# Performance work log

Measured on AMD Instinct MI355X. Metric: run time of the kernel, lower is better.

The kernel has to match this reference:

```python
import jax, jax.numpy as jnp
import numpy as np

B = 8
S_MAX = 1024
H = 12
HD = 64
D = H * HD
DFF = 4 * D
NEG = -1.0e9  # matches Triton kernel's -1000000000.0 mask value


def _layernorm(x, g, b, eps=1e-6):
    mu = jnp.mean(x, axis=-1, keepdims=True)
    var = jnp.mean((x - mu) ** 2, axis=-1, keepdims=True)
    return (x - mu) * jax.lax.rsqrt(var + eps) * g + b


def setup_inputs() -> dict:
    key = jax.random.key(0)
    ks = jax.random.split(key, 12)
    lengths = np.array([1024, 896, 768, 640, 896, 1024, 512, 384], dtype=np.int32)
    assert lengths.max() <= S_MAX and len(lengths) == B
    total = int(lengths.sum())  # 6144
    cu = jnp.asarray(np.concatenate([[0], np.cumsum(lengths)]), dtype=jnp.int32)
    s = 0.02
    return {
        "x": jax.random.normal(ks[0], (total, D), jnp.float32),
        "cu_seqlens": cu,
        "g1": jnp.ones((D,), jnp.float32),
        "beta1": jnp.zeros((D,), jnp.float32),
        "Wqkv": jax.random.normal(ks[1], (D, 3 * D), jnp.float32) * s,
        "bqkv": jnp.zeros((3 * D,), jnp.float32),
        "Wo": jax.random.normal(ks[2], (D, D), jnp.float32) * s,
        "bo": jnp.zeros((D,), jnp.float32),
        "g2": jnp.ones((D,), jnp.float32),
        "beta2": jnp.zeros((D,), jnp.float32),
        "W1": jax.random.normal(ks[3], (D, DFF), jnp.float32) * s,
        "b_fc1": jnp.zeros((DFF,), jnp.float32),
        "W2": jax.random.normal(ks[4], (DFF, D), jnp.float32) * s,
        "b_fc2": jnp.zeros((D,), jnp.float32),
    }


def _ragged_attention(q, k, v, cu_seqlens):
    # q,k,v: [Total, H, HD] packed ragged sequences; cu_seqlens: [B+1] int32
    total = q.shape[0]
    lens = cu_seqlens[1:] - cu_seqlens[:-1]                      # [B]
    s = jnp.arange(S_MAX)
    pad_idx = cu_seqlens[:-1, None] + jnp.minimum(s[None, :], lens[:, None] - 1)  # [B,S]
    valid = s[None, :] < lens[:, None]                           # [B,S]
    qp = q[pad_idx]                                              # [B,S,H,HD]
    kp = k[pad_idx]
    vp = v[pad_idx]
    scale = 1.0 / jnp.sqrt(jnp.float32(HD))
    scores = jnp.einsum("bqhd,bkhd->bhqk", qp, kp) * scale      # [B,H,S,S]
    scores = jnp.where(valid[:, None, None, :], scores, NEG)     # mask invalid keys
    p = jax.nn.softmax(scores, axis=-1)
    op = jnp.einsum("bhqk,bkhd->bqhd", p, vp)                   # [B,S,H,HD]
    # repack to [Total, H, HD]
    tok = jnp.arange(total)
    seg = jnp.searchsorted(cu_seqlens, tok, side="right") - 1    # sequence id per token
    pos = tok - cu_seqlens[seg]
    return op[seg, pos]


def _forward(x, cu_seqlens, g1, beta1, Wqkv, bqkv, Wo, bo, g2, beta2, W1, b_fc1, W2, b_fc2):
    total = x.shape[0]
    qkv = (_layernorm(x, g1, beta1) @ Wqkv + bqkv).reshape(total, 3, H, HD)
    q, k, v = qkv[:, 0], qkv[:, 1], qkv[:, 2]
    attn = _ragged_attention(q, k, v, cu_seqlens).reshape(total, D)
    x = x + (attn @ Wo + bo)                                     # proj_drop/ls1/drop_path identity (eval)
    h = _layernorm(x, g2, beta2)
    m = jax.nn.gelu(h @ W1 + b_fc1, approximate=False)
    return x + (m @ W2 + b_fc2)


def reference(x, cu_seqlens, g1, beta1, Wqkv, bqkv, Wo, bo, g2, beta2, W1, b_fc1, W2, b_fc2):
    return _forward(x, cu_seqlens, g1, beta1, Wqkv, bqkv, Wo, bo, g2, beta2, W1, b_fc1, W2, b_fc2)
```

## Files before the change

kernel.cpp:

```cpp
#include <hip/hip_runtime.h>
#include <hip/hip_bf16.h>
#include <stdint.h>
#include <string.h>

#define D_MODEL 768
#define H_HEADS 12
#define HD_ 64
#define N_QKV 2304

typedef __bf16 bf16x8 __attribute__((ext_vector_type(8)));
typedef float f32x4 __attribute__((ext_vector_type(4)));

__device__ __forceinline__ unsigned short f2bfbits(float f) {
  union { float f; unsigned u; } x; x.f = f;
  unsigned r = x.u + 0x7fffu + ((x.u >> 16) & 1u);
  return (unsigned short)(r >> 16);
}

__device__ __forceinline__ unsigned pk2(float a, float b) {
  union { float f; unsigned u; } x, y; x.f = a; y.f = b;
  return ((x.u + 0x8000u) >> 16) | ((y.u + 0x8000u) & 0xffff0000u);
}

__global__ void transpose_w(const float* __restrict__ in, unsigned short* __restrict__ out,
                            int R, int C) {
  __shared__ float tile[32][33];
  int c0 = blockIdx.x * 32, r0 = blockIdx.y * 32;
  int tx = threadIdx.x, ty = threadIdx.y;
#pragma unroll
  for (int i = 0; i < 32; i += 8)
    tile[ty + i][tx] = in[(size_t)(r0 + ty + i) * C + c0 + tx];
  __syncthreads();
#pragma unroll
  for (int i = 0; i < 32; i += 8)
    out[(size_t)(c0 + ty + i) * R + r0 + tx] = f2bfbits(tile[tx][ty + i]);
}

__global__ void transpose_v(const unsigned short* __restrict__ qkv,
                            unsigned short* __restrict__ vT, int M) {
  __shared__ unsigned short tile[32][33];
  int t0 = blockIdx.x * 32, c0 = blockIdx.y * 32;
  int tx = threadIdx.x, ty = threadIdx.y;
#pragma unroll
  for (int i = 0; i < 32; i += 8)
    tile[ty + i][tx] = qkv[(size_t)(t0 + ty + i) * N_QKV + 1536 + c0 + tx];
  __syncthreads();
  int t = t0 + tx;
  int c = t & 63;
  int kp = ((c >> 5) << 5) | (((c >> 2) & 3) << 3) | (((c >> 4) & 1) << 2) | (c & 3);
  size_t col = (size_t)(t & ~63) + kp;
#pragma unroll
  for (int i = 0; i < 32; i += 8)
    vT[(size_t)(c0 + ty + i) * M + col] = tile[tx][ty + i];
}

__global__ void ln_bf16(const float* __restrict__ x, const float* __restrict__ g,
                        const float* __restrict__ be, unsigned short* __restrict__ out) {
  int row = blockIdx.x;
  const float* xr = x + (size_t)row * D_MODEL;
  int t = threadIdx.x;
  float v0 = xr[t], v1 = xr[t + 256], v2 = xr[t + 512];
  float s = v0 + v1 + v2;
  float s2 = v0 * v0 + v1 * v1 + v2 * v2;
#pragma unroll
  for (int off = 32; off > 0; off >>= 1) {
    s += __shfl_down(s, off, 64);
    s2 += __shfl_down(s2, off, 64);
  }
  __shared__ float red[8];
  int w = t >> 6, lane = t & 63;
  if (lane == 0) { red[w] = s; red[w + 4] = s2; }
  __syncthreads();
  if (t == 0) {
    float a = red[0] + red[1] + red[2] + red[3];
    float b = red[4] + red[5] + red[6] + red[7];
    red[0] = a * (1.0f / 768.0f);
    red[4] = b * (1.0f / 768.0f);
  }
  __syncthreads();
  float mu = red[0];
  float var = red[4] - mu * mu;
  float rs = rsqrtf(var + 1e-6f);
  unsigned short* orow = out + (size_t)row * D_MODEL;
  orow[t]       = f2bfbits((v0 - mu) * rs * g[t]       + be[t]);
  orow[t + 256] = f2bfbits((v1 - mu) * rs * g[t + 256] + be[t + 256]);
  orow[t + 512] = f2bfbits((v2 - mu) * rs * g[t + 512] + be[t + 512]);
}

template <int EPI>
__global__ void __launch_bounds__(256, 3)
gemm_rs(const unsigned short* __restrict__ A,
        const unsigned short* __restrict__ Bt,
        const float* __restrict__ bias,
        const float* __restrict__ res,
        void* __restrict__ outv,
        int M, int N, int K) {
  __shared__ unsigned short lA[2][128 * 32];
  __shared__ unsigned short lB[2][128 * 32];
  int tid = threadIdx.x;
  int w = tid >> 6, lane = tid & 63;
  int id = blockIdx.x;
  int nn = N >> 7, bandM = (M >> 7) >> 3;
  int xcd = id & 7, s = id >> 3;
  int mt = xcd * bandM + s / nn;
  int nt = s - (s / nn) * nn;
  int m0 = mt * 128, n0 = nt * 128;
  int wm = (w >> 1) * 64, wn = (w & 1) * 64;
  f32x4 acc[4][4];
#pragma unroll
  for (int i = 0; i < 4; i++)
#pragma unroll
    for (int j = 0; j < 4; j++) acc[i][j] = (f32x4){0.f, 0.f, 0.f, 0.f};

  int sr = tid >> 2, sc = tid & 3;
  const unsigned short* gA = A + (size_t)(m0 + sr) * K + sc * 8;
  const unsigned short* gB = Bt + (size_t)(n0 + sr) * K + sc * 8;
  int wOff = sr * 64 + ((((sr >> 1) & 3) ^ sc) * 16);
  int fm = lane & 15, fg = lane >> 4;

  uint4 pA0, pA1, pB0, pB1;
  uint4 qA0, qA1, qB0, qB1;

  int nk = K >> 5;
  pA0 = *(const uint4*)(gA);
  pA1 = *(const uint4*)(gA + (size_t)64 * K);
  pB0 = *(const uint4*)(gB);
  pB1 = *(const uint4*)(gB + (size_t)64 * K);
  qA0 = *(const uint4*)(gA + 32);
  qA1 = *(const uint4*)(gA + (size_t)64 * K + 32);
  qB0 = *(const uint4*)(gB + 32);
  qB1 = *(const uint4*)(gB + (size_t)64 * K + 32);

  for (int k = 0; k < nk; k += 2) {
    {
      char* la = (char*)&lA[0][0];
      char* lb = (char*)&lB[0][0];
      *(uint4*)(la + wOff) = pA0;
      *(uint4*)(la + wOff + 4096) = pA1;
      *(uint4*)(lb + wOff) = pB0;
      *(uint4*)(lb + wOff + 4096) = pB1;
      if (k + 2 < nk) {
        int k0 = (k + 2) * 32;
        pA0 = *(const uint4*)(gA + k0);
        pA1 = *(const uint4*)(gA + (size_t)64 * K + k0);
        pB0 = *(const uint4*)(gB + k0);
        pB1 = *(const uint4*)(gB + (size_t)64 * K + k0);
      }
      asm volatile("s_waitcnt lgkmcnt(0)\ns_barrier" ::: "memory");
      bf16x8 af[4], bfr[4];
#pragma unroll
      for (int i = 0; i < 4; i++) {
        int rr = wm + i * 16 + fm;
        af[i] = *(const bf16x8*)(la + rr * 64 + ((((rr >> 1) & 3) ^ fg) * 16));
      }
#pragma unroll
      for (int j = 0; j < 4; j++) {
        int rr = wn + j * 16 + fm;
        bfr[j] = *(const bf16x8*)(lb + rr * 64 + ((((rr >> 1) & 3) ^ fg) * 16));
      }
#pragma unroll
      for (int i = 0; i < 4; i++)
#pragma unroll
        for (int j = 0; j < 4; j++)
          acc[i][j] = __builtin_amdgcn_mfma_f32_16x16x32_bf16(af[i], bfr[j], acc[i][j], 0, 0, 0);
    }
    {
      char* la = (char*)&lA[1][0];
      char* lb = (char*)&lB[1][0];
      *(uint4*)(la + wOff) = qA0;
      *(uint4*)(la + wOff + 4096) = qA1;
      *(uint4*)(lb + wOff) = qB0;
      *(uint4*)(lb + wOff + 4096) = qB1;
      if (k + 3 < nk) {
        int k0 = (k + 3) * 32;
        qA0 = *(const uint4*)(gA + k0);
        qA1 = *(const uint4*)(gA + (size_t)64 * K + k0);
        qB0 = *(const uint4*)(gB + k0);
        qB1 = *(const uint4*)(gB + (size_t)64 * K + k0);
      }
      asm volatile("s_waitcnt lgkmcnt(0)\ns_barrier" ::: "memory");
      bf16x8 af[4], bfr[4];
#pragma unroll
      for (int i = 0; i < 4; i++) {
        int rr = wm + i * 16 + fm;
        af[i] = *(const bf16x8*)(la + rr * 64 + ((((rr >> 1) & 3) ^ fg) * 16));
      }
#pragma unroll
      for (int j = 0; j < 4; j++) {
        int rr = wn + j * 16 + fm;
        bfr[j] = *(const bf16x8*)(lb + rr * 64 + ((((rr >> 1) & 3) ^ fg) * 16));
      }
#pragma unroll
      for (int i = 0; i < 4; i++)
#pragma unroll
        for (int j = 0; j < 4; j++)
          acc[i][j] = __builtin_amdgcn_mfma_f32_16x16x32_bf16(af[i], bfr[j], acc[i][j], 0, 0, 0);
    }
  }

  int er = (lane >> 4) * 4, ec = lane & 15;
#pragma unroll
  for (int i = 0; i < 4; i++) {
#pragma unroll
    for (int j = 0; j < 4; j++) {
      int n = n0 + wn + j * 16 + ec;
      float bv = bias[n];
#pragma unroll
      for (int r = 0; r < 4; r++) {
        int m = m0 + wm + i * 16 + er + r;
        float v = acc[i][j][r] + bv;
        if (EPI == 1) {
          v += res[(size_t)m * N + n];
          ((float*)outv)[(size_t)m * N + n] = v;
        } else {
          if (EPI == 2) v = 0.5f * v * (1.0f + erff(v * 0.70710678118f));
          ((unsigned short*)outv)[(size_t)m * N + n] = f2bfbits(v);
        }
      }
    }
  }
}

__global__ void attn_flash4(const unsigned short* __restrict__ qkv,
                            const unsigned short* __restrict__ vT,
                            const int* __restrict__ cu,
                            unsigned short* __restrict__ out, int M) {
  int id = blockIdx.x;
  int qc = id / 96;
  int bh = id - qc * 96;
  int b = bh / 12, h = bh - b * 12;
  int tok0 = cu[b];
  int len = cu[b + 1] - tok0;
  if (qc * 128 >= len) return;

  __shared__ unsigned short lK[2][64 * 64];
  __shared__ unsigned short lVT[2][64 * 64];

  int tid = threadIdx.x, w = tid >> 6, lane = tid & 63;
  int fm = lane & 15, fg = lane >> 4;
  int xm = fm & 7;
  int qbase = qc * 128 + w * 32;

  bf16x8 qf[2][2];
#pragma unroll
  for (int qs = 0; qs < 2; qs++)
#pragma unroll
    for (int kh = 0; kh < 2; kh++)
      qf[qs][kh] = *(const bf16x8*)(qkv + (size_t)(tok0 + qbase + qs * 16 + fm) * N_QKV +
                                    h * 64 + kh * 32 + fg * 8);

  f32x4 Oacc[2][4];
#pragma unroll
  for (int qs = 0; qs < 2; qs++)
#pragma unroll
    for (int dt = 0; dt < 4; dt++) Oacc[qs][dt] = (f32x4){0.f, 0.f, 0.f, 0.f};
  float lrow[2] = {0.f, 0.f};
  const float C2 = 0.18033688011112042f;

  int sr = tid >> 3, sp = tid & 7, sl = sp ^ (sr & 7);
  const unsigned short* kg0 = qkv + D_MODEL + h * 64 + sl * 8;
  const unsigned short* vg0 = vT + (size_t)(h * 64 + sr) * M + tok0 + sl * 8;

  uint4 rk0, rk1, rv0, rv1;
  auto gload = [&](int kt) {
    rk0 = *(const uint4*)(kg0 + (size_t)(tok0 + kt + sr) * N_QKV);
    rk1 = *(const uint4*)(kg0 + (size_t)(tok0 + kt + sr + 32) * N_QKV);
    rv0 = *(const uint4*)(vg0 + kt);
    rv1 = *(const uint4*)(vg0 + (size_t)32 * M + kt);
  };

  int nkt = len >> 6;
  gload(0);
  for (int kt = 0; kt < nkt; kt++) {
    int cur = kt & 1;
    *(uint4*)((char*)&lK[cur][0] + tid * 16) = rk0;
    *(uint4*)((char*)&lK[cur][0] + tid * 16 + 4096) = rk1;
    *(uint4*)((char*)&lVT[cur][0] + tid * 16) = rv0;
    *(uint4*)((char*)&lVT[cur][0] + tid * 16 + 4096) = rv1;
    if (kt + 1 < nkt) gload((kt + 1) * 64);
    asm volatile("s_waitcnt lgkmcnt(0)\ns_barrier" ::: "memory");

    f32x4 s[2][4];
#pragma unroll
    for (int qs = 0; qs < 2; qs++)
#pragma unroll
      for (int t = 0; t < 4; t++) s[qs][t] = (f32x4){0.f, 0.f, 0.f, 0.f};
#pragma unroll
    for (int t = 0; t < 4; t++) {
      bf16x8 kf0 = *(const bf16x8*)&lK[cur][(t * 16 + fm) * 64 + ((fg ^ xm) * 8)];
      bf16x8 kf1 = *(const bf16x8*)&lK[cur][(t * 16 + fm) * 64 + (((4 + fg) ^ xm) * 8)];
#pragma unroll
      for (int qs = 0; qs < 2; qs++) {
        s[qs][t] = __builtin_amdgcn_mfma_f32_16x16x32_bf16(kf0, qf[qs][0], s[qs][t], 0, 0, 0);
        s[qs][t] = __builtin_amdgcn_mfma_f32_16x16x32_bf16(kf1, qf[qs][1], s[qs][t], 0, 0, 0);
      }
    }

    union { bf16x8 v; unsigned u[4]; } af[2][2];
#pragma unroll
    for (int qs = 0; qs < 2; qs++) {
      float ssum = 0.f;
#pragma unroll
      for (int t = 0; t < 4; t++) {
#pragma unroll
        for (int r = 0; r < 4; r++) {
          float p = exp2f(s[qs][t][r] * C2);
          s[qs][t][r] = p;
          ssum += p;
        }
      }
      lrow[qs] += ssum;
      af[qs][0].u[0] = pk2(s[qs][0][0], s[qs][0][1]);
      af[qs][0].u[1] = pk2(s[qs][0][2], s[qs][0][3]);
      af[qs][0].u[2] = pk2(s[qs][1][0], s[qs][1][1]);
      af[qs][0].u[3] = pk2(s[qs][1][2], s[qs][1][3]);
      af[qs][1].u[0] = pk2(s[qs][2][0], s[qs][2][1]);
      af[qs][1].u[1] = pk2(s[qs][2][2], s[qs][2][3]);
      af[qs][1].u[2] = pk2(s[qs][3][0], s[qs][3][1]);
      af[qs][1].u[3] = pk2(s[qs][3][2], s[qs][3][3]);
    }

#pragma unroll
    for (int dt = 0; dt < 4; dt++) {
      bf16x8 vf0 = *(const bf16x8*)&lVT[cur][(dt * 16 + fm) * 64 + ((fg ^ xm) * 8)];
      bf16x8 vf1 = *(const bf16x8*)&lVT[cur][(dt * 16 + fm) * 64 + (((4 + fg) ^ xm) * 8)];
#pragma unroll
      for (int qs = 0; qs < 2; qs++) {
        Oacc[qs][dt] = __builtin_amdgcn_mfma_f32_16x16x32_bf16(af[qs][0].v, vf0, Oacc[qs][dt], 0, 0, 0);
        Oacc[qs][dt] = __builtin_amdgcn_mfma_f32_16x16x32_bf16(af[qs][1].v, vf1, Oacc[qs][dt], 0, 0, 0);
      }
    }
  }

#pragma unroll
  for (int qs = 0; qs < 2; qs++) {
    lrow[qs] += __shfl_xor(lrow[qs], 16, 64);
    lrow[qs] += __shfl_xor(lrow[qs], 32, 64);
    float inv = 1.0f / lrow[qs];
    float ir[4];
#pragma unroll
    for (int r = 0; r < 4; r++) ir[r] = __shfl(inv, fg * 4 + r, 64);
#pragma unroll
    for (int dt = 0; dt < 4; dt++)
#pragma unroll
      for (int r = 0; r < 4; r++)
        out[(size_t)(tok0 + qbase + qs * 16 + fg * 4 + r) * D_MODEL + h * 64 + dt * 16 + fm] =
            f2bfbits(Oacc[qs][dt][r] * ir[r]);
  }
}

extern "C" void kernel_launch(void* const* d_in, const int* in_sizes, int n_in,
                              void* d_out, int out_size, void* d_ws, size_t ws_size,
                              hipStream_t stream) {
  const float* x    = (const float*)d_in[0];
  const int* cu     = (const int*)d_in[1];
  const float* g1   = (const float*)d_in[2];
  const float* be1  = (const float*)d_in[3];
  const float* Wqkv = (const float*)d_in[4];
  const float* bqkv = (const float*)d_in[5];
  const float* Wo   = (const float*)d_in[6];
  const float* bo   = (const float*)d_in[7];
  const float* g2   = (const float*)d_in[8];
  const float* be2  = (const float*)d_in[9];
  const float* W1   = (const float*)d_in[10];
  const float* bfc1 = (const float*)d_in[11];
  const float* W2   = (const float*)d_in[12];
  const float* bfc2 = (const float*)d_in[13];
  float* out = (float*)d_out;
  int M = in_sizes[0] / D_MODEL;

  unsigned short* WqkvT = (unsigned short*)d_ws;
  unsigned short* WoT   = WqkvT + 2304 * 768;
  unsigned short* W1T   = WoT + 768 * 768;
  unsigned short* W2T   = W1T + 3072 * 768;
  unsigned short* bufA  = W2T + 768 * 3072;
  float* x1             = (float*)(bufA + (size_t)M * D_MODEL);
  unsigned short* qkvb  = (unsigned short*)(x1 + (size_t)M * D_MODEL);
  unsigned short* vT = (unsigned short*)x1;

  dim3 b32(32, 8);
  transpose_w<<<dim3(2304 / 32, 768 / 32), b32, 0, stream>>>(Wqkv, WqkvT, 768, 2304);
  transpose_w<<<dim3(768 / 32, 768 / 32), b32, 0, stream>>>(Wo, WoT, 768, 768);
  transpose_w<<<dim3(3072 / 32, 768 / 32), b32, 0, stream>>>(W1, W1T, 768, 3072);
  transpose_w<<<dim3(768 / 32, 3072 / 32), b32, 0, stream>>>(W2, W2T, 3072, 768);

  ln_bf16<<<M, 256, 0, stream>>>(x, g1, be1, bufA);
  gemm_rs<0><<<(2304 / 128) * (M / 128), 256, 0, stream>>>(bufA, WqkvT, bqkv, nullptr, qkvb, M, 2304, 768);
  transpose_v<<<dim3(M / 32, 768 / 32), b32, 0, stream>>>(qkvb, vT, M);
  attn_flash4<<<8 * 96, 256, 0, stream>>>(qkvb, vT, cu, bufA, M);
  gemm_rs<1><<<(768 / 128) * (M / 128), 256, 0, stream>>>(bufA, WoT, bo, x, x1, M, 768, 768);
  ln_bf16<<<M, 256, 0, stream>>>(x1, g2, be2, bufA);
  gemm_rs<2><<<(3072 / 128) * (M / 128), 256, 0, stream>>>(bufA, W1T, bfc1, nullptr, qkvb, M, 3072, 768);
  gemm_rs<1><<<(768 / 128) * (M / 128), 256, 0, stream>>>(qkvb, W2T, bfc2, x1, out, M, 768, 3072);
}
```

Baseline: 343.9 us.

## Add 256x256-tile GEMM with direct global-to-LDS loads for QKV and FC1

Adds a new GEMM kernel using 256x256 output tiles with 512 threads, loading tiles straight from global memory into LDS via global_load_lds, double-buffering across split K halves, and grouping blocks into M bands per XCD. The QKV and FC1 projections switch to it from the older 128x128 kernel. The aim is more data reuse per tile, less load-instruction overhead, and better L2 locality. The trade-off is fewer blocks (M=6144 gives 216 and 288 blocks), which raises tail and occupancy risk, plus heavier register use for the 8x4 accumulator array.

```diff
diff --git a/kernel.cpp b/kernel.cpp
--- a/kernel.cpp
+++ b/kernel.cpp
@@ -20,6 +20,12 @@
 __device__ __forceinline__ unsigned pk2(float a, float b) {
   union { float f; unsigned u; } x, y; x.f = a; y.f = b;
   return ((x.u + 0x8000u) >> 16) | ((y.u + 0x8000u) & 0xffff0000u);
+}
+
+__device__ __forceinline__ void gload_lds16(const void* g, void* l) {
+  __builtin_amdgcn_global_load_lds(
+      (const __attribute__((address_space(1))) unsigned int*)g,
+      (__attribute__((address_space(3))) unsigned int*)l, 16, 0, 0);
 }
 
 __global__ void transpose_w(const float* __restrict__ in, unsigned short* __restrict__ out,
@@ -221,6 +227,163 @@
   }
 }
 
+#define BAR_() asm volatile("s_barrier" ::: "memory")
+#define BARLGKM_() asm volatile("s_barrier\ns_waitcnt lgkmcnt(0)" ::: "memory")
+
+template <int EPI>
+__global__ void __launch_bounds__(512, 2)
+gemm256(const unsigned short* __restrict__ A,
+        const unsigned short* __restrict__ Bt,
+        const float* __restrict__ bias,
+        void* __restrict__ outv,
+        int M, int N, int K) {
+  __shared__ unsigned short sA[2][2][256 * 32];
+  __shared__ unsigned short sB[2][2][256 * 32];
+  const int tid = threadIdx.x;
+  const int w = tid >> 6, lane = tid & 63;
+  const int fm = lane & 15, fg = lane >> 4;
+
+  const int id = blockIdx.x;
+  const int nn = N >> 8, bandM = (M >> 8) >> 3;
+  const int xcd = id & 7, sblk = id >> 3;
+  const int mt = xcd * bandM + sblk / nn;
+  const int nt = sblk - (sblk / nn) * nn;
+  const int m0 = mt << 8, n0 = nt << 8;
+  const int wm = (w >> 2) * 128, wn = (w & 3) * 64;
+
+  f32x4 acc[8][4];
+#pragma unroll
+  for (int i = 0; i < 8; ++i)
+#pragma unroll
+    for (int j = 0; j < 4; ++j) acc[i][j] = (f32x4){0.f, 0.f, 0.f, 0.f};
+
+  int offA0[4], offA1[4], offB[4];
+#pragma unroll
+  for (int i = 0; i < 4; ++i) {
+    int ra = wm + i * 16 + fm;
+    offA0[i] = ra * 64 + ((((ra >> 1) & 3) ^ fg) * 16);
+    int rb = wm + 64 + i * 16 + fm;
+    offA1[i] = rb * 64 + ((((rb >> 1) & 3) ^ fg) * 16);
+    int rc = wn + i * 16 + fm;
+    offB[i] = rc * 64 + ((((rc >> 1) & 3) ^ fg) * 16);
+  }
+
+  const int r0 = w * 32 + (lane >> 2);
+  const int cg = (lane & 3) ^ ((r0 >> 1) & 3);
+  const unsigned short* gA0 = A + (size_t)(m0 + r0) * K + cg * 8;
+  const unsigned short* gA1 = gA0 + (size_t)16 * K;
+  const unsigned short* gB0 = Bt + (size_t)(n0 + r0) * K + cg * 8;
+  const unsigned short* gB1 = gB0 + (size_t)16 * K;
+  const int lo0 = w * 2048, lo1 = w * 2048 + 1024;
+  const int NT = K >> 6;
+
+  auto stA = [&](int kt, int ks, int buf) {
+    int kk = kt < NT ? kt : NT - 1;
+    int off = kk * 64 + ks * 32;
+    char* base = (char*)&sA[buf][ks][0];
+    gload_lds16(gA0 + off, base + lo0);
+    gload_lds16(gA1 + off, base + lo1);
+  };
+  auto stB = [&](int kt, int ks, int buf) {
+    int kk = kt < NT ? kt : NT - 1;
+    int off = kk * 64 + ks * 32;
+    char* base = (char*)&sB[buf][ks][0];
+    gload_lds16(gB0 + off, base + lo0);
+    gload_lds16(gB1 + off, base + lo1);
+  };
+
+  stB(0, 0, 0); stB(0, 1, 0); stA(0, 0, 0); stA(0, 1, 0);
+  asm volatile("s_waitcnt vmcnt(4)" ::: "memory");
+  stB(1, 0, 1); stB(1, 1, 1); stA(1, 0, 1);
+  asm volatile("s_waitcnt vmcnt(6)" ::: "memory");
+  BAR_();
+
+  for (int t = 0; t < NT; ++t) {
+    const int cur = t & 1;
+    const char* As0 = (const char*)&sA[cur][0][0];
+    const char* As1 = (const char*)&sA[cur][1][0];
+    const char* Bs0 = (const char*)&sB[cur][0][0];
+    const char* Bs1 = (const char*)&sB[cur][1][0];
+    bf16x8 a[4], b0[4], b1[4];
+
+#pragma unroll
+    for (int i = 0; i < 4; ++i) a[i] = *(const bf16x8*)(As0 + offA0[i]);
+#pragma unroll
+    for (int j = 0; j < 4; ++j) b0[j] = *(const bf16x8*)(Bs0 + offB[j]);
+#pragma unroll
+    for (int j = 0; j < 4; ++j) b1[j] = *(const bf16x8*)(Bs1 + offB[j]);
+    stA(t + 1, 1, (t + 1) & 1);
+    BARLGKM_();
+    __builtin_amdgcn_s_setprio(1);
+#pragma unroll
+    for (int i = 0; i < 4; ++i)
+#pragma unroll
+      for (int j = 0; j < 4; ++j)
+        acc[i][j] = __builtin_amdgcn_mfma_f32_16x16x32_bf16(a[i], b0[j], acc[i][j], 0, 0, 0);
+    __builtin_amdgcn_s_setprio(0);
+    BAR_();
+
+#pragma unroll
+    for (int i = 0; i < 4; ++i) a[i] = *(const bf16x8*)(As0 + offA1[i]);
+    stB(t + 2, 0, cur);
+    BARLGKM_();
+    __builtin_amdgcn_s_setprio(1);
+#pragma unroll
+    for (int i = 0; i < 4; ++i)
+#pragma unroll
+      for (int j = 0; j < 4; ++j)
+        acc[4 + i][j] = __builtin_amdgcn_mfma_f32_16x16x32_bf16(a[i], b0[j], acc[4 + i][j], 0, 0, 0);
+    __builtin_amdgcn_s_setprio(0);
+    BAR_();
+
+#pragma unroll
+    for (int i = 0; i < 4; ++i) a[i] = *(const bf16x8*)(As1 + offA0[i]);
+    stB(t + 2, 1, cur);
+    BARLGKM_();
+    __builtin_amdgcn_s_setprio(1);
+#pragma unroll
+    for (int i = 0; i < 4; ++i)
+#pragma unroll
+      for (int j = 0; j < 4; ++j)
+        acc[i][j] = __builtin_amdgcn_mfma_f32_16x16x32_bf16(a[i], b1[j], acc[i][j], 0, 0, 0);
+    __builtin_amdgcn_s_setprio(0);
+    BAR_();
+
+#pragma unroll
+    for (int i = 0; i < 4; ++i) a[i] = *(const bf16x8*)(As1 + offA1[i]);
+    stA(t + 2, 0, cur);
+    asm volatile("s_waitcnt vmcnt(6)" ::: "memory");
+    BARLGKM_();
+    __builtin_amdgcn_s_setprio(1);
+#pragma unroll
+    for (int i = 0; i < 4; ++i)
+#pragma unroll
+      for (int j = 0; j < 4; ++j)
+        acc[4 + i][j] = __builtin_amdgcn_mfma_f32_16x16x32_bf16(a[i], b1[j], acc[4 + i][j], 0, 0, 0);
+    __builtin_amdgcn_s_setprio(0);
+    BAR_();
+  }
+
+  asm volatile("s_waitcnt vmcnt(0)" ::: "memory");
+
+  const int er = fg * 4, ec = fm;
+#pragma unroll
+  for (int i = 0; i < 8; ++i) {
+#pragma unroll
+    for (int j = 0; j < 4; ++j) {
+      int n = n0 + wn + j * 16 + ec;
+      float bv = bias[n];
+#pragma unroll
+      for (int r = 0; r < 4; ++r) {
+        int m = m0 + wm + i * 16 + er + r;
+        float v = acc[i][j][r] + bv;
+        if (EPI == 2) v = 0.5f * v * (1.0f + erff(v * 0.70710678118f));
+        ((unsigned short*)outv)[(size_t)m * N + n] = f2bfbits(v);
+      }
+    }
+  }
+}
+
 __global__ void attn_flash4(const unsigned short* __restrict__ qkv,
                             const unsigned short* __restrict__ vT,
                             const int* __restrict__ cu,
@@ -385,11 +548,11 @@
   transpose_w<<<dim3(768 / 32, 3072 / 32), b32, 0, stream>>>(W2, W2T, 3072, 768);
 
   ln_bf16<<<M, 256, 0, stream>>>(x, g1, be1, bufA);
-  gemm_rs<0><<<(2304 / 128) * (M / 128), 256, 0, stream>>>(bufA, WqkvT, bqkv, nullptr, qkvb, M, 2304, 768);
+  gemm256<0><<<(2304 / 256) * (M / 256), 512, 0, stream>>>(bufA, WqkvT, bqkv, qkvb, M, 2304, 768);
   transpose_v<<<dim3(M / 32, 768 / 32), b32, 0, stream>>>(qkvb, vT, M);
   attn_flash4<<<8 * 96, 256, 0, stream>>>(qkvb, vT, cu, bufA, M);
   gemm_rs<1><<<(768 / 128) * (M / 128), 256, 0, stream>>>(bufA, WoT, bo, x, x1, M, 768, 768);
   ln_bf16<<<M, 256, 0, stream>>>(x1, g2, be2, bufA);
-  gemm_rs<2><<<(3072 / 128) * (M / 128), 256, 0, stream>>>(bufA, W1T, bfc1, nullptr, qkvb, M, 3072, 768);
+  gemm256<2><<<(3072 / 256) * (M / 256), 512, 0, stream>>>(bufA, W1T, bfc1, qkvb, M, 3072, 768);
   gemm_rs<1><<<(768 / 128) * (M / 128), 256, 0, stream>>>(qkvb, W2T, bfc2, x1, out, M, 768, 3072);
 }
```

Result: slower. 412.1 us (+19.8%).
